# Optimization experiments

Hardware: AMD Instinct MI355X
Metric: run time of the kernel (lower is better)

## Reference

```python
import jax, jax.numpy as jnp
import numpy as np

POOL_LIST = (1, 2, 4)  # pyramid levels -> 1x1, 2x2, 4x4 bins


def _spp_mix(x, pool_list=POOL_LIST):
    """Spatial pyramid pooling, pool_type='mix' (max + mean), channels_last.

    x: (B, H, W, C) -> (B, sum(p*p for p in pool_list) * C)
    Matches the original TF loop ordering: for each level, outer loop over
    bin columns (jy), inner loop over bin rows (ix).
    """
    B, H, W, C = x.shape
    outs = []
    for p in pool_list:
        wr, wc = H // p, W // p  # window rows/cols (floor div, as in original)
        # crop to covered region, then split into p x p bins in one reshape
        xs = x[:, :p * wr, :p * wc, :].reshape(B, p, wr, p, wc, C)
        # mix = max + mean over each window
        v = xs.max(axis=(2, 4)) + xs.mean(axis=(2, 4))  # (B, pr, pc, C)
        # original appends in (jy outer, ix inner) order -> transpose rows/cols
        v = jnp.transpose(v, (0, 2, 1, 3)).reshape(B, p * p * C)
        outs.append(v)
    return jnp.concatenate(outs, axis=-1)


def setup_inputs() -> dict:
    key = jax.random.key(0)
    x = jax.random.normal(key, (32, 64, 64, 512), dtype=jnp.float32)
    return {"x": x}


def reference(x) -> jnp.ndarray:
    return _spp_mix(x)
```

## Files before the change

kernel.cpp:

```cpp
#include <hip/hip_runtime.h>
#include <math.h>


#define B_ 32
#define HW_ 64
#define C_ 512
#define CVEC 128

__device__ __forceinline__ float4 f4max(float4 a, float4 b) {
    return make_float4(fmaxf(a.x, b.x), fmaxf(a.y, b.y),
                       fmaxf(a.z, b.z), fmaxf(a.w, b.w));
}
__device__ __forceinline__ float4 f4add(float4 a, float4 b) {
    return make_float4(a.x + b.x, a.y + b.y, a.z + b.z, a.w + b.w);
}
__device__ __forceinline__ float4 f4mix(float4 m, float4 s, float inv) {
    return make_float4(m.x + s.x * inv, m.y + s.y * inv,
                       m.z + s.z * inv, m.w + s.w * inv);
}

__global__ __launch_bounds__(256) void spp_bins_kernel(
    const float4* __restrict__ x,
    float4* __restrict__ maxbuf,
    float4* __restrict__ sumbuf)
{
    const int blk  = blockIdx.x;
    const int b    = blk >> 4;
    const int bin  = blk & 15;
    const int br   = bin >> 2;
    const int bc   = bin & 3;
    const int tid  = threadIdx.x;
    const int cg   = tid & (CVEC - 1);
    const int half = tid >> 7;

    const int base = ((b * HW_ + br * 16) * HW_ + bc * 16) * CVEC + cg;

    float4 mx = make_float4(-INFINITY, -INFINITY, -INFINITY, -INFINITY);
    float4 sm = make_float4(0.f, 0.f, 0.f, 0.f);

    #pragma unroll 8
    for (int k = 0; k < 128; ++k) {
        const int s = (half << 7) + k;
        const int i = s >> 4;
        const int j = s & 15;
        const float4 v = x[base + (i * HW_ + j) * CVEC];
        mx = f4max(mx, v);
        sm = f4add(sm, v);
    }

    __shared__ float4 smax[CVEC];
    __shared__ float4 ssum[CVEC];
    if (half == 1) { smax[cg] = mx; ssum[cg] = sm; }
    __syncthreads();
    if (half == 0) {
        mx = f4max(mx, smax[cg]);
        sm = f4add(sm, ssum[cg]);
        const int o = (b * 16 + bin) * CVEC + cg;
        maxbuf[o] = mx;
        sumbuf[o] = sm;
    }
}

__global__ __launch_bounds__(256) void spp_agg_kernel(
    const float4* __restrict__ maxbuf,
    const float4* __restrict__ sumbuf,
    float4* __restrict__ out)
{
    const int idx = blockIdx.x * 256 + threadIdx.x;
    const int b   = idx >> 7;
    const int cg  = idx & (CVEC - 1);

    float4 m[16], s[16];
    #pragma unroll
    for (int bin = 0; bin < 16; ++bin) {
        const int o = (b * 16 + bin) * CVEC + cg;
        m[bin] = maxbuf[o];
        s[bin] = sumbuf[o];
    }

    const int row = b * (21 * CVEC);

    #pragma unroll
    for (int br = 0; br < 4; ++br) {
        #pragma unroll
        for (int bc = 0; bc < 4; ++bc) {
            const int bin = br * 4 + bc;
            out[row + 5 * CVEC + (bc * 4 + br) * CVEC + cg] =
                f4mix(m[bin], s[bin], 1.0f / 256.0f);
        }
    }

    float4 m2[4], s2[4];
    #pragma unroll
    for (int pr = 0; pr < 2; ++pr) {
        #pragma unroll
        for (int pc = 0; pc < 2; ++pc) {
            const int b00 = (2 * pr) * 4 + (2 * pc);
            float4 mm = f4max(f4max(m[b00], m[b00 + 1]),
                              f4max(m[b00 + 4], m[b00 + 5]));
            float4 ss = f4add(f4add(s[b00], s[b00 + 1]),
                              f4add(s[b00 + 4], s[b00 + 5]));
            m2[pr * 2 + pc] = mm;
            s2[pr * 2 + pc] = ss;
            out[row + CVEC + (pc * 2 + pr) * CVEC + cg] =
                f4mix(mm, ss, 1.0f / 1024.0f);
        }
    }

    float4 mm = f4max(f4max(m2[0], m2[1]), f4max(m2[2], m2[3]));
    float4 ss = f4add(f4add(s2[0], s2[1]), f4add(s2[2], s2[3]));
    out[row + cg] = f4mix(mm, ss, 1.0f / 4096.0f);
}

extern "C" void kernel_launch(void* const* d_in, const int* in_sizes, int n_in,
                              void* d_out, int out_size, void* d_ws, size_t ws_size,
                              hipStream_t stream) {
    const float4* x = (const float4*)d_in[0];
    float* ws = (float*)d_ws;
    float4* maxbuf = (float4*)ws;
    float4* sumbuf = (float4*)(ws + B_ * 16 * C_);
    float4* out = (float4*)d_out;

    spp_bins_kernel<<<B_ * 16, 256, 0, stream>>>(x, maxbuf, sumbuf);
    spp_agg_kernel<<<(B_ * CVEC) / 256, 256, 0, stream>>>(maxbuf, sumbuf, out);
}
```

Measured before the change: 354.0 us.

## Split each bin reduction across 8 row-slices with 1024-thread blocks and tree reduce

After: 352.7 us. No clear change (-0.4%).

```diff
diff --git a/kernel.cpp b/kernel.cpp
--- a/kernel.cpp
+++ b/kernel.cpp
@@ -19,97 +19,109 @@
                        m.z + s.z * inv, m.w + s.w * inv);
 }
 
-__global__ __launch_bounds__(256) void spp_bins_kernel(
+__global__ __launch_bounds__(1024, 8) void spp_bins_kernel(
     const float4* __restrict__ x,
     float4* __restrict__ maxbuf,
-    float4* __restrict__ sumbuf)
+    float4* __restrict__ sumbuf,
+    float4* __restrict__ out)
 {
-    const int blk  = blockIdx.x;
-    const int b    = blk >> 4;
-    const int bin  = blk & 15;
-    const int br   = bin >> 2;
-    const int bc   = bin & 3;
-    const int tid  = threadIdx.x;
-    const int cg   = tid & (CVEC - 1);
-    const int half = tid >> 7;
+    const int blk   = blockIdx.x;
+    const int b     = blk >> 4;
+    const int bin   = blk & 15;
+    const int br    = bin >> 2;
+    const int bc    = bin & 3;
+    const int tid   = threadIdx.x;
+    const int cg    = tid & (CVEC - 1);
+    const int slice = tid >> 7;
 
-    const int base = ((b * HW_ + br * 16) * HW_ + bc * 16) * CVEC + cg;
+    const int base =
+        ((b * HW_ + br * 16 + slice * 2) * HW_ + bc * 16) * CVEC + cg;
+    const float4* p = x + base;
 
     float4 mx = make_float4(-INFINITY, -INFINITY, -INFINITY, -INFINITY);
     float4 sm = make_float4(0.f, 0.f, 0.f, 0.f);
 
     #pragma unroll 8
-    for (int k = 0; k < 128; ++k) {
-        const int s = (half << 7) + k;
-        const int i = s >> 4;
-        const int j = s & 15;
-        const float4 v = x[base + (i * HW_ + j) * CVEC];
+    for (int k = 0; k < 32; ++k) {
+        const int r = k >> 4;
+        const int j = k & 15;
+        const float4 v = p[(r * HW_ + j) * CVEC];
         mx = f4max(mx, v);
         sm = f4add(sm, v);
     }
 
-    __shared__ float4 smax[CVEC];
-    __shared__ float4 ssum[CVEC];
-    if (half == 1) { smax[cg] = mx; ssum[cg] = sm; }
+    __shared__ float4 smax[8][CVEC];
+    __shared__ float4 ssum[8][CVEC];
+    smax[slice][cg] = mx;
+    ssum[slice][cg] = sm;
     __syncthreads();
-    if (half == 0) {
-        mx = f4max(mx, smax[cg]);
-        sm = f4add(sm, ssum[cg]);
+
+    #pragma unroll
+    for (int off = 4; off >= 1; off >>= 1) {
+        if (slice < off) {
+            mx = f4max(mx, smax[slice + off][cg]);
+            sm = f4add(sm, ssum[slice + off][cg]);
+            if (off > 1) { smax[slice][cg] = mx; ssum[slice][cg] = sm; }
+        }
+        __syncthreads();
+    }
+
+    if (slice == 0) {
         const int o = (b * 16 + bin) * CVEC + cg;
         maxbuf[o] = mx;
         sumbuf[o] = sm;
+        const int row = b * (21 * CVEC);
+        out[row + 5 * CVEC + (bc * 4 + br) * CVEC + cg] =
+            f4mix(mx, sm, 1.0f / 256.0f);
     }
 }
 
-__global__ __launch_bounds__(256) void spp_agg_kernel(
+__global__ __launch_bounds__(256) void spp_l12_kernel(
     const float4* __restrict__ maxbuf,
     const float4* __restrict__ sumbuf,
     float4* __restrict__ out)
 {
-    const int idx = blockIdx.x * 256 + threadIdx.x;
-    const int b   = idx >> 7;
-    const int cg  = idx & (CVEC - 1);
+    const int b   = blockIdx.x >> 3;
+    const int cgc = blockIdx.x & 7;
+    const int tid = threadIdx.x;
+    const int bin = tid >> 4;
+    const int cgi = tid & 15;
+    const int cg  = cgc * 16 + cgi;
 
-    float4 m[16], s[16];
-    #pragma unroll
-    for (int bin = 0; bin < 16; ++bin) {
-        const int o = (b * 16 + bin) * CVEC + cg;
-        m[bin] = maxbuf[o];
-        s[bin] = sumbuf[o];
-    }
+    __shared__ float4 sm_[16][16];
+    __shared__ float4 ss_[16][16];
+    __shared__ float4 sm2[4][16];
+    __shared__ float4 ss2[4][16];
+
+    const int o = (b * 16 + bin) * CVEC + cg;
+    sm_[bin][cgi] = maxbuf[o];
+    ss_[bin][cgi] = sumbuf[o];
+    __syncthreads();
 
     const int row = b * (21 * CVEC);
 
-    #pragma unroll
-    for (int br = 0; br < 4; ++br) {
-        #pragma unroll
-        for (int bc = 0; bc < 4; ++bc) {
-            const int bin = br * 4 + bc;
-            out[row + 5 * CVEC + (bc * 4 + br) * CVEC + cg] =
-                f4mix(m[bin], s[bin], 1.0f / 256.0f);
-        }
+    if (tid < 64) {
+        const int l2 = tid >> 4;
+        const int pr = l2 >> 1, pc = l2 & 1;
+        const int b00 = (2 * pr) * 4 + (2 * pc);
+        float4 mm = f4max(f4max(sm_[b00][cgi], sm_[b00 + 1][cgi]),
+                          f4max(sm_[b00 + 4][cgi], sm_[b00 + 5][cgi]));
+        float4 ss = f4add(f4add(ss_[b00][cgi], ss_[b00 + 1][cgi]),
+                          f4add(ss_[b00 + 4][cgi], ss_[b00 + 5][cgi]));
+        sm2[l2][cgi] = mm;
+        ss2[l2][cgi] = ss;
+        out[row + CVEC + (pc * 2 + pr) * CVEC + cg] =
+            f4mix(mm, ss, 1.0f / 1024.0f);
     }
+    __syncthreads();
 
-    float4 m2[4], s2[4];
-    #pragma unroll
-    for (int pr = 0; pr < 2; ++pr) {
-        #pragma unroll
-        for (int pc = 0; pc < 2; ++pc) {
-            const int b00 = (2 * pr) * 4 + (2 * pc);
-            float4 mm = f4max(f4max(m[b00], m[b00 + 1]),
-                              f4max(m[b00 + 4], m[b00 + 5]));
-            float4 ss = f4add(f4add(s[b00], s[b00 + 1]),
-                              f4add(s[b00 + 4], s[b00 + 5]));
-            m2[pr * 2 + pc] = mm;
-            s2[pr * 2 + pc] = ss;
-            out[row + CVEC + (pc * 2 + pr) * CVEC + cg] =
-                f4mix(mm, ss, 1.0f / 1024.0f);
-        }
+    if (tid < 16) {
+        float4 mm = f4max(f4max(sm2[0][tid], sm2[1][tid]),
+                          f4max(sm2[2][tid], sm2[3][tid]));
+        float4 ss = f4add(f4add(ss2[0][tid], ss2[1][tid]),
+                          f4add(ss2[2][tid], ss2[3][tid]));
+        out[row + cgc * 16 + tid] = f4mix(mm, ss, 1.0f / 4096.0f);
     }
-
-    float4 mm = f4max(f4max(m2[0], m2[1]), f4max(m2[2], m2[3]));
-    float4 ss = f4add(f4add(s2[0], s2[1]), f4add(s2[2], s2[3]));
-    out[row + cg] = f4mix(mm, ss, 1.0f / 4096.0f);
 }
 
 extern "C" void kernel_launch(void* const* d_in, const int* in_sizes, int n_in,
@@ -121,6 +133,6 @@
     float4* sumbuf = (float4*)(ws + B_ * 16 * C_);
     float4* out = (float4*)d_out;
 
-    spp_bins_kernel<<<B_ * 16, 256, 0, stream>>>(x, maxbuf, sumbuf);
-    spp_agg_kernel<<<(B_ * CVEC) / 256, 256, 0, stream>>>(maxbuf, sumbuf, out);
+    spp_bins_kernel<<<B_ * 16, 1024, 0, stream>>>(x, maxbuf, sumbuf, out);
+    spp_l12_kernel<<<B_ * 8, 256, 0, stream>>>(maxbuf, sumbuf, out);
 }
```
